# Optimization experiments

Measured on AMD Instinct MI355X. Metric: run time of the kernel, lower is better.

The kernel has to match this reference:

```python
import jax, jax.numpy as jnp
import numpy as np

EMBED_DIM = 2048
NUM_HEADS = 32
NUM_KV_HEADS = 8
HEAD_DIM = EMBED_DIM // NUM_HEADS  # 64
KV_DIM = HEAD_DIM * NUM_KV_HEADS   # 512
Q_PER_KV = NUM_HEADS // NUM_KV_HEADS  # 4


def setup_inputs() -> dict:
    key = jax.random.key(0)
    ks = jax.random.split(key, 9)
    s = 1.0 / np.sqrt(EMBED_DIM)
    x = jax.random.normal(ks[0], (2, 2048, EMBED_DIM), dtype=jnp.float32)
    Wq = jax.random.uniform(ks[1], (EMBED_DIM, EMBED_DIM), jnp.float32, -s, s)
    bq = jax.random.uniform(ks[2], (EMBED_DIM,), jnp.float32, -s, s)
    Wk = jax.random.uniform(ks[3], (KV_DIM, EMBED_DIM), jnp.float32, -s, s)
    bk = jax.random.uniform(ks[4], (KV_DIM,), jnp.float32, -s, s)
    Wv = jax.random.uniform(ks[5], (KV_DIM, EMBED_DIM), jnp.float32, -s, s)
    bv = jax.random.uniform(ks[6], (KV_DIM,), jnp.float32, -s, s)
    Wo = jax.random.uniform(ks[7], (EMBED_DIM, EMBED_DIM), jnp.float32, -s, s)
    bo = jax.random.uniform(ks[8], (EMBED_DIM,), jnp.float32, -s, s)
    return {"x": x, "Wq": Wq, "bq": bq, "Wk": Wk, "bk": bk,
            "Wv": Wv, "bv": bv, "Wo": Wo, "bo": bo}


def reference(x, Wq, bq, Wk, bk, Wv, bv, Wo, bo):
    B, S, E = x.shape
    # projections (torch Linear: x @ W.T + b)
    q = x @ Wq.T + bq                       # [B,S,E]
    k = x @ Wk.T + bk                       # [B,S,KV_DIM]
    v = x @ Wv.T + bv
    # [B, num_kv, q_per_kv, S, D] and [B, num_kv, S, D] -- GQA grouping
    # avoids repeat_interleave duplication while computing identical math
    q = q.reshape(B, S, NUM_KV_HEADS, Q_PER_KV, HEAD_DIM).transpose(0, 2, 3, 1, 4)
    k = k.reshape(B, S, NUM_KV_HEADS, HEAD_DIM).transpose(0, 2, 1, 3)
    v = v.reshape(B, S, NUM_KV_HEADS, HEAD_DIM).transpose(0, 2, 1, 3)
    scale = 1.0 / np.sqrt(HEAD_DIM).astype(np.float32)
    scores = jnp.einsum('bgqsd,bgtd->bgqst', q, k) * scale  # [B,G,Qpk,S,S]
    causal = jnp.triu(jnp.ones((S, S), dtype=bool), k=1)
    scores = jnp.where(causal, jnp.float32(-jnp.inf), scores)
    attn = jax.nn.softmax(scores, axis=-1)
    out = jnp.einsum('bgqst,bgtd->bgqsd', attn, v)          # [B,G,Qpk,S,D]
    # back to [B,S,E]: head order matches repeat_interleave (kv-major)
    out = out.transpose(0, 3, 1, 2, 4).reshape(B, S, E)
    return out @ Wo.T + bo
```

## Files before the change

kernel.cpp:

```cpp
#include <hip/hip_runtime.h>
#include <stdint.h>

#define EMBED  2048
#define SEQ    2048
#define BATCH  2
#define NHEADS 32
#define NKV    8
#define HDIM   64
#define KVD    512
#define MTOT   (BATCH*SEQ)
#define QKVN   (EMBED + 2*KVD)

typedef __bf16 bf16x8 __attribute__((ext_vector_type(8)));
typedef float  f32x4  __attribute__((ext_vector_type(4)));
typedef float  f32x8v __attribute__((ext_vector_type(8)));
typedef float  f32x2v __attribute__((ext_vector_type(2)));
typedef float  f32x16 __attribute__((ext_vector_type(16)));

#define QSCALE 0.18033688f
#define M2     11.541560f

static __device__ __forceinline__ unsigned short f2bf(float f) {
    union { float f; unsigned int u; } v; v.f = f;
    return (unsigned short)((v.u + 0x7fffu + ((v.u >> 16) & 1u)) >> 16);
}

static __device__ __forceinline__ void gload_lds16(const void* g, void* l) {
    __builtin_amdgcn_global_load_lds(
        (const __attribute__((address_space(1))) void*)g,
        (__attribute__((address_space(3))) void*)l, 16, 0, 0);
}

template<int N> static __device__ __forceinline__ void waitvm() {
    if constexpr (N == 2) asm volatile("s_waitcnt vmcnt(2)" ::: "memory");
    else if constexpr (N == 3) asm volatile("s_waitcnt vmcnt(3)" ::: "memory");
    else asm volatile("s_waitcnt vmcnt(4)" ::: "memory");
}

__global__ void cast_f32_bf16(const float* __restrict__ in,
                              unsigned short* __restrict__ out, int n4) {
    int i = blockIdx.x * blockDim.x + threadIdx.x;
    int stride = gridDim.x * blockDim.x;
    for (; i < n4; i += stride) {
        float4 f = reinterpret_cast<const float4*>(in)[i];
        ushort4 o;
        o.x = f2bf(f.x); o.y = f2bf(f.y); o.z = f2bf(f.z); o.w = f2bf(f.w);
        reinterpret_cast<ushort4*>(out)[i] = o;
    }
}

__global__ void pack_bias(const float* __restrict__ bq, const float* __restrict__ bk,
                          const float* __restrict__ bv, float* __restrict__ o) {
    int i = blockIdx.x * blockDim.x + threadIdx.x;
    if (i < EMBED) o[i] = bq[i];
    else if (i < EMBED + KVD) o[i] = bk[i - EMBED];
    else if (i < QKVN) o[i] = bv[i - EMBED - KVD];
}

template<int WM, bool OUT_BF16>
__global__ __launch_bounds__(512, 1)
void gemm8p(const unsigned short* __restrict__ A,
            const unsigned short* __restrict__ B,
            const float* __restrict__ bias,
            void* __restrict__ C, int M, int N, int K)
{
    constexpr int BM    = WM * 32;
    constexpr int ASZ   = BM * 128;
    constexpr int BSZ   = 256 * 128;
    constexpr int AHALF = ASZ / 2;
    constexpr int AL    = AHALF / 8192;
    constexpr int BUFSZ = ASZ + BSZ;

    __shared__ __align__(16) char lds[2 * BUFSZ];

    const int tid = threadIdx.x;
    const int l   = tid & 63;
    const int w   = tid >> 6;
    const int wr  = w >> 2, wc = w & 3;
    const int lr15 = l & 15;
    const int lkb  = (l >> 4) * 16;

    const int nwg = gridDim.x;
    const int cpx = nwg >> 3;
    const int bid = blockIdx.x;
    const int swz = (bid & 7) * cpx + (bid >> 3);
    const int NMB = M / BM;
    const int m0  = (swz % NMB) * BM;
    const int n0  = (swz / NMB) * 256;

    unsigned offA[2][AL], dA[2][AL];
#pragma unroll
    for (int q = 0; q < 2; ++q)
#pragma unroll
        for (int j = 0; j < AL; ++j) {
            int L  = q * AHALF + (tid + j * 512) * 16;
            int R  = L >> 7;
            int cb = (L & 127) ^ ((R & 7) << 4);
            int lrow;
            if constexpr (WM == 8) lrow = ((R >> 6) & 1) * 128 + (R >> 7) * 64 + (R & 63);
            else                   lrow = ((R >> 5) & 1) * 64  + (R >> 6) * 32 + (R & 31);
            offA[q][j] = (unsigned)((m0 + lrow) * K * 2 + cb);
            dA[q][j]   = (unsigned)L;
        }
    unsigned offB[2][2], dB[2][2];
#pragma unroll
    for (int q = 0; q < 2; ++q)
#pragma unroll
        for (int j = 0; j < 2; ++j) {
            int L  = q * 16384 + (tid + j * 512) * 16;
            int R  = L >> 7;
            int cb = (L & 127) ^ ((R & 7) << 4);
            int lrow = ((R >> 5) & 3) * 64 + (R >> 7) * 32 + (R & 31);
            offB[q][j] = (unsigned)((n0 + lrow) * K * 2 + cb);
            dB[q][j]   = (unsigned)(ASZ + L);
        }

#define STAGE_A(q, bw, ku) { _Pragma("unroll") \
    for (int j_ = 0; j_ < AL; ++j_) \
        gload_lds16((const char*)A + offA[q][j_] + (unsigned)(ku) * 128u, (bw) + dA[q][j_]); }
#define STAGE_B(q, bw, ku) { _Pragma("unroll") \
    for (int j_ = 0; j_ < 2; ++j_) \
        gload_lds16((const char*)B + offB[q][j_] + (unsigned)(ku) * 128u, (bw) + dB[q][j_]); }

    auto rdA = [&](const char* br, int mi, int kk) -> bf16x8 {
        int row;
        if constexpr (WM == 8) row = (mi >> 2) * 128 + wr * 64 + (mi & 3) * 16 + lr15;
        else                   row = (mi >> 1) * 64  + wr * 32 + (mi & 1) * 16 + lr15;
        int byte = (row * 128 + kk * 64 + lkb) ^ ((row & 7) << 4);
        return *reinterpret_cast<const bf16x8*>(br + byte);
    };
    auto rdB = [&](const char* br, int ni, int kk) -> bf16x8 {
        int row  = (ni >> 1) * 128 + wc * 32 + (ni & 1) * 16 + lr15;
        int byte = (row * 128 + kk * 64 + lkb) ^ ((row & 7) << 4);
        return *reinterpret_cast<const bf16x8*>(br + ASZ + byte);
    };

    f32x4 acc[WM][4] = {};
    bf16x8 afr[WM / 2][2], bf0[2][2], bf1[2][2];

    STAGE_A(0, lds, 0); STAGE_B(0, lds, 0); STAGE_B(1, lds, 0); STAGE_A(1, lds, 0);
    waitvm<2 + AL>();
    __builtin_amdgcn_s_barrier();

    const int NKT = K >> 6;
    for (int u = 0; u < NKT; ++u) {
        char* br = lds + (u & 1) * BUFSZ;
        char* bw = lds + ((u & 1) ^ 1) * BUFSZ;
        const bool pf = (u + 1 < NKT);
        const int  ku = u + 1;

        if (pf) STAGE_A(0, bw, ku);
#pragma unroll
        for (int mi = 0; mi < WM / 2; ++mi)
#pragma unroll
            for (int kk = 0; kk < 2; ++kk) afr[mi][kk] = rdA(br, mi, kk);
#pragma unroll
        for (int ni = 0; ni < 2; ++ni)
#pragma unroll
            for (int kk = 0; kk < 2; ++kk) bf0[ni][kk] = rdB(br, ni, kk);
        __builtin_amdgcn_s_barrier();
        __builtin_amdgcn_s_setprio(1);
#pragma unroll
        for (int mi = 0; mi < WM / 2; ++mi)
#pragma unroll
            for (int ni = 0; ni < 2; ++ni)
#pragma unroll
                for (int kk = 0; kk < 2; ++kk)
                    acc[mi][ni] = __builtin_amdgcn_mfma_f32_16x16x32_bf16(afr[mi][kk], bf0[ni][kk], acc[mi][ni], 0, 0, 0);
        __builtin_amdgcn_s_setprio(0);
        waitvm<2 * AL>();
        __builtin_amdgcn_s_barrier();

        if (pf) STAGE_B(0, bw, ku);
#pragma unroll
        for (int ni = 0; ni < 2; ++ni)
#pragma unroll
            for (int kk = 0; kk < 2; ++kk) bf1[ni][kk] = rdB(br, 2 + ni, kk);
        __builtin_amdgcn_s_barrier();
        __builtin_amdgcn_s_setprio(1);
#pragma unroll
        for (int mi = 0; mi < WM / 2; ++mi)
#pragma unroll
            for (int ni = 0; ni < 2; ++ni)
#pragma unroll
                for (int kk = 0; kk < 2; ++kk)
                    acc[mi][2 + ni] = __builtin_amdgcn_mfma_f32_16x16x32_bf16(afr[mi][kk], bf1[ni][kk], acc[mi][2 + ni], 0, 0, 0);
        __builtin_amdgcn_s_setprio(0);
        waitvm<AL + 2>();
        __builtin_amdgcn_s_barrier();

        if (pf) STAGE_B(1, bw, ku);
#pragma unroll
        for (int mi = 0; mi < WM / 2; ++mi)
#pragma unroll
            for (int kk = 0; kk < 2; ++kk) afr[mi][kk] = rdA(br, WM / 2 + mi, kk);
        __builtin_amdgcn_s_barrier();
        __builtin_amdgcn_s_setprio(1);
#pragma unroll
        for (int mi = 0; mi < WM / 2; ++mi)
#pragma unroll
            for (int ni = 0; ni < 2; ++ni)
#pragma unroll
                for (int kk = 0; kk < 2; ++kk)
                    acc[WM / 2 + mi][ni] = __builtin_amdgcn_mfma_f32_16x16x32_bf16(afr[mi][kk], bf0[ni][kk], acc[WM / 2 + mi][ni], 0, 0, 0);
        __builtin_amdgcn_s_setprio(0);
        __builtin_amdgcn_s_barrier();

        if (pf) STAGE_A(1, bw, ku);
        __builtin_amdgcn_s_barrier();
        __builtin_amdgcn_s_setprio(1);
#pragma unroll
        for (int mi = 0; mi < WM / 2; ++mi)
#pragma unroll
            for (int ni = 0; ni < 2; ++ni)
#pragma unroll
                for (int kk = 0; kk < 2; ++kk)
                    acc[WM / 2 + mi][2 + ni] = __builtin_amdgcn_mfma_f32_16x16x32_bf16(afr[mi][kk], bf1[ni][kk], acc[WM / 2 + mi][2 + ni], 0, 0, 0);
        __builtin_amdgcn_s_setprio(0);
        waitvm<2 + AL>();
        __builtin_amdgcn_s_barrier();
    }
#undef STAGE_A
#undef STAGE_B

    float bv[4];
#pragma unroll
    for (int ni = 0; ni < 4; ++ni) bv[ni] = bias[n0 + wc * 64 + ni * 16 + lr15];
#pragma unroll
    for (int mi = 0; mi < WM; ++mi)
#pragma unroll
        for (int ni = 0; ni < 4; ++ni)
#pragma unroll
            for (int r = 0; r < 4; ++r) {
                int row = m0 + wr * (WM * 16) + mi * 16 + (l >> 4) * 4 + r;
                int col = n0 + wc * 64 + ni * 16 + lr15;
                float v = acc[mi][ni][r] + bv[ni];
                if constexpr (OUT_BF16)
                    ((unsigned short*)C)[(size_t)row * N + col] = f2bf(v);
                else
                    ((float*)C)[(size_t)row * N + col] = v;
            }
}

static __device__ __forceinline__ bf16x8 pack_frag(float p0, float p1, float p2, float p3,
                                                   float p4, float p5, float p6, float p7) {
    unsigned int w0, w1, w2, w3;
    asm("v_cvt_pk_bf16_f32 %0, %1, %2" : "=v"(w0) : "v"(p0), "v"(p1));
    asm("v_cvt_pk_bf16_f32 %0, %1, %2" : "=v"(w1) : "v"(p2), "v"(p3));
    asm("v_cvt_pk_bf16_f32 %0, %1, %2" : "=v"(w2) : "v"(p4), "v"(p5));
    asm("v_cvt_pk_bf16_f32 %0, %1, %2" : "=v"(w3) : "v"(p6), "v"(p7));
    asm("v_permlane32_swap_b32 %0, %1" : "+v"(w0), "+v"(w2));
    asm("v_permlane32_swap_b32 %0, %1" : "+v"(w1), "+v"(w3));
    union { unsigned int u[4]; bf16x8 v; } uu;
    uu.u[0] = w0; uu.u[1] = w1; uu.u[2] = w2; uu.u[3] = w3;
    return uu.v;
}

static __device__ __forceinline__ float hsum32(f32x16 a, f32x16 b) {
    f32x16 t = a + b;
    f32x8v u = __builtin_shufflevector(t, t, 0,1,2,3,4,5,6,7)
             + __builtin_shufflevector(t, t, 8,9,10,11,12,13,14,15);
    f32x4 v4 = __builtin_shufflevector(u, u, 0,1,2,3)
             + __builtin_shufflevector(u, u, 4,5,6,7);
    f32x2v v2 = __builtin_shufflevector(v4, v4, 0,1)
              + __builtin_shufflevector(v4, v4, 2,3);
    return v2[0] + v2[1];
}

static __device__ __forceinline__ void attn_tile(
    const char* __restrict__ KsBuf, const char* __restrict__ VtBuf,
    const bf16x8* qf, int q, int t0, bool diag,
    f32x16& acc0, f32x16& acc1, float& l_run,
    int lq, int hi)
{
    f32x16 s0 = {}, s1 = {};
    __builtin_amdgcn_s_setprio(1);
#pragma unroll
    for (int ks = 0; ks < 4; ++ks) {
        const int colb = (ks * 16 + hi * 8) * 2;
        int a0 = (lq * 128 + colb) ^ ((lq & 7) << 4);
        bf16x8 kf0 = *reinterpret_cast<const bf16x8*>(KsBuf + a0);
        s0 = __builtin_amdgcn_mfma_f32_32x32x16_bf16(kf0, qf[ks], s0, 0, 0, 0);
        int r1 = 32 + lq;
        int a1 = (r1 * 128 + colb) ^ ((r1 & 7) << 4);
        bf16x8 kf1 = *reinterpret_cast<const bf16x8*>(KsBuf + a1);
        s1 = __builtin_amdgcn_mfma_f32_32x32x16_bf16(kf1, qf[ks], s1, 0, 0, 0);
    }
    __builtin_amdgcn_s_setprio(0);

    if (diag) {
#pragma unroll
        for (int r = 0; r < 16; ++r) {
            int tg = t0 + (r & 3) + 8 * (r >> 2) + 4 * hi;
            if (tg > q) s0[r] = -1e30f;
            if (tg + 32 > q) s1[r] = -1e30f;
        }
    }

    s0 = s0 - M2;
    s1 = s1 - M2;
#pragma unroll
    for (int r = 0; r < 16; ++r) {
        s0[r] = __builtin_amdgcn_exp2f(s0[r]);
        s1[r] = __builtin_amdgcn_exp2f(s1[r]);
    }

    float rs = hsum32(s0, s1);
    l_run += rs + __shfl_xor(rs, 32);

    bf16x8 pa[4];
    pa[0] = pack_frag(s0[0], s0[1], s0[2], s0[3], s0[4], s0[5], s0[6], s0[7]);
    pa[1] = pack_frag(s0[8], s0[9], s0[10], s0[11], s0[12], s0[13], s0[14], s0[15]);
    pa[2] = pack_frag(s1[0], s1[1], s1[2], s1[3], s1[4], s1[5], s1[6], s1[7]);
    pa[3] = pack_frag(s1[8], s1[9], s1[10], s1[11], s1[12], s1[13], s1[14], s1[15]);

    __builtin_amdgcn_s_setprio(1);
#pragma unroll
    for (int ks = 0; ks < 4; ++ks) {
        const int colb = (ks * 16 + hi * 8) * 2;
        int a0 = (lq * 128 + colb) ^ ((lq & 7) << 4);
        bf16x8 vf0 = *reinterpret_cast<const bf16x8*>(VtBuf + a0);
        acc0 = __builtin_amdgcn_mfma_f32_32x32x16_bf16(pa[ks], vf0, acc0, 0, 0, 0);
        int d1 = 32 + lq;
        int a1 = (d1 * 128 + colb) ^ ((d1 & 7) << 4);
        bf16x8 vf1 = *reinterpret_cast<const bf16x8*>(VtBuf + a1);
        acc1 = __builtin_amdgcn_mfma_f32_32x32x16_bf16(pa[ks], vf1, acc1, 0, 0, 0);
    }
    __builtin_amdgcn_s_setprio(0);
}

__global__ __launch_bounds__(512)
void gqa_attn(const unsigned short* __restrict__ qkv,
              unsigned short* __restrict__ ctx)
{
    __shared__ __align__(16) unsigned short Ks[2][64 * 64];
    __shared__ __align__(16) unsigned short Vt[2][64 * 64];

    const int bid = blockIdx.x;
    const int gb  = (bid & 7) * 2 + ((bid >> 3) & 1);
    const int pr  = bid >> 4;
    const int g   = gb & 7;
    const int b   = gb >> 3;
    const int qtA = pr, qtB = 31 - pr;
    const int NT  = qtB + 1;

    const int tid = threadIdx.x;
    const int l   = tid & 63;
    const int w   = tid >> 6;
    const int hi  = l >> 5;
    const int lq  = l & 31;

    const int h   = g * 4 + (w >> 1);
    const int q0A = qtA * 64 + (w & 1) * 32;
    const int q0B = qtB * 64 + (w & 1) * 32;
    const size_t rowb = (size_t)b * SEQ;
    const int kbase = EMBED + g * HDIM;
    const int vbase = EMBED + KVD + g * HDIM;

    bf16x8 qfA[4], qfB[4];
    {
        const char* qa = (const char*)qkv + ((rowb + q0A + lq) * QKVN + (size_t)h * HDIM) * 2;
        const char* qb = (const char*)qkv + ((rowb + q0B + lq) * QKVN + (size_t)h * HDIM) * 2;
#pragma unroll
        for (int ks = 0; ks < 4; ++ks) {
            bf16x8 ta = *reinterpret_cast<const bf16x8*>(qa + (ks * 16 + hi * 8) * 2);
            bf16x8 tb = *reinterpret_cast<const bf16x8*>(qb + (ks * 16 + hi * 8) * 2);
#pragma unroll
            for (int j = 0; j < 8; ++j) {
                ta[j] = (__bf16)((float)ta[j] * QSCALE);
                tb[j] = (__bf16)((float)tb[j] * QSCALE);
            }
            qfA[ks] = ta; qfB[ks] = tb;
        }
    }

    f32x16 accA0 = {}, accA1 = {}, accB0 = {}, accB1 = {};
    float lA = 0.0f, lB = 0.0f;

    const int Lk   = tid << 4;
    const int Tk   = Lk ^ (((Lk >> 7) & 7) << 4);
    const int krow = Tk >> 7, koff = Tk & 127;

    {
        const char* kp = (const char*)qkv + ((rowb + krow) * QKVN + kbase) * 2 + koff;
        gload_lds16(kp, (char*)Ks[0] + Lk);
        const char* vp = (const char*)qkv + ((rowb + l) * QKVN + vbase + w * 8) * 2;
        uint4 vv = *reinterpret_cast<const uint4*>(vp);
        const unsigned short* e = (const unsigned short*)&vv;
#pragma unroll
        for (int j = 0; j < 8; ++j) {
            int d = w * 8 + j;
            int byteoff = (d * 128 + l * 2) ^ ((d & 7) << 4);
            *(unsigned short*)((char*)Vt[0] + byteoff) = e[j];
        }
    }
    __syncthreads();

    for (int kt = 0; kt < NT; ++kt) {
        const int cur = kt & 1;
        const int t0  = kt * 64;
        const bool haveNext = (kt + 1 < NT);
        uint4 vn;
        if (haveNext) {
            const char* kp = (const char*)qkv + ((rowb + t0 + 64 + krow) * QKVN + kbase) * 2 + koff;
            gload_lds16(kp, (char*)Ks[cur ^ 1] + Lk);
            const char* vp = (const char*)qkv + ((rowb + t0 + 64 + l) * QKVN + vbase + w * 8) * 2;
            vn = *reinterpret_cast<const uint4*>(vp);
        }

        attn_tile((const char*)Ks[cur], (const char*)Vt[cur], qfB, q0B + lq, t0,
                  kt == qtB, accB0, accB1, lB, lq, hi);
        if (kt <= qtA)
            attn_tile((const char*)Ks[cur], (const char*)Vt[cur], qfA, q0A + lq, t0,
                      kt == qtA, accA0, accA1, lA, lq, hi);

        if (haveNext) {
            const unsigned short* e = (const unsigned short*)&vn;
#pragma unroll
            for (int j = 0; j < 8; ++j) {
                int d = w * 8 + j;
                int byteoff = (d * 128 + l * 2) ^ ((d & 7) << 4);
                *(unsigned short*)((char*)Vt[cur ^ 1] + byteoff) = e[j];
            }
            __syncthreads();
        }
    }

#pragma unroll
    for (int r = 0; r < 16; ++r) {
        int qr  = (r & 3) + 8 * (r >> 2) + 4 * hi;
        int col = h * HDIM + lq;
        float lrB = __shfl(lB, qr);
        size_t rowB = rowb + q0B + qr;
        ctx[rowB * EMBED + col]      = f2bf(accB0[r] / lrB);
        ctx[rowB * EMBED + col + 32] = f2bf(accB1[r] / lrB);
        float lrA = __shfl(lA, qr);
        size_t rowA = rowb + q0A + qr;
        ctx[rowA * EMBED + col]      = f2bf(accA0[r] / lrA);
        ctx[rowA * EMBED + col + 32] = f2bf(accA1[r] / lrA);
    }
}

extern "C" void kernel_launch(void* const* d_in, const int* in_sizes, int n_in,
                              void* d_out, int out_size, void* d_ws, size_t ws_size,
                              hipStream_t stream) {
    (void)in_sizes; (void)n_in; (void)out_size; (void)ws_size;
    const float* x  = (const float*)d_in[0];
    const float* Wq = (const float*)d_in[1];
    const float* bq = (const float*)d_in[2];
    const float* Wk = (const float*)d_in[3];
    const float* bk = (const float*)d_in[4];
    const float* Wv = (const float*)d_in[5];
    const float* bv = (const float*)d_in[6];
    const float* Wo = (const float*)d_in[7];
    const float* bo = (const float*)d_in[8];
    float* out = (float*)d_out;

    char* ws = (char*)d_ws;
    unsigned short* xb    = (unsigned short*)(ws);
    unsigned short* Wqkvb = (unsigned short*)(ws + 16777216);
    unsigned short* Wob   = (unsigned short*)(ws + 29360128);
    float*          bqkv  = (float*)         (ws + 37748736);
    unsigned short* QKVb  = (unsigned short*)(ws + 37761024);
    unsigned short* ctx   = (unsigned short*)(ws + 62926848);

    cast_f32_bf16<<<2048, 256, 0, stream>>>(x,  xb,                        (MTOT * EMBED) / 4);
    cast_f32_bf16<<<1024, 256, 0, stream>>>(Wq, Wqkvb,                     (EMBED * EMBED) / 4);
    cast_f32_bf16<<<256,  256, 0, stream>>>(Wk, Wqkvb + EMBED * EMBED,     (KVD * EMBED) / 4);
    cast_f32_bf16<<<256,  256, 0, stream>>>(Wv, Wqkvb + (EMBED + KVD) * EMBED, (KVD * EMBED) / 4);
    cast_f32_bf16<<<1024, 256, 0, stream>>>(Wo, Wob,                       (EMBED * EMBED) / 4);
    pack_bias<<<12, 256, 0, stream>>>(bq, bk, bv, bqkv);

    gemm8p<8, true><<<dim3(192), 512, 0, stream>>>(
        xb, Wqkvb, bqkv, QKVb, MTOT, QKVN, EMBED);

    gqa_attn<<<dim3(256), 512, 0, stream>>>(QKVb, ctx);

    gemm8p<4, false><<<dim3(256), 512, 0, stream>>>(
        ctx, Wob, bo, out, MTOT, EMBED, EMBED);
}
```

Measured before the change: 195.9 us.

## Split attention blocks into head pairs with 256 threads and 512 blocks

Each attention block now covers two of the four query heads in a KV group instead of all four. It runs 4 waves instead of 8, and the grid doubles to 512 blocks. Each thread loads twice as much of the K and V tiles, and the launch bounds target 4 blocks per CU. The aim is better CU coverage and occupancy on the large GPU, at the cost of loading each K/V tile twice per group.

```diff
diff --git a/kernel.cpp b/kernel.cpp
--- a/kernel.cpp
+++ b/kernel.cpp
@@ -329,7 +329,7 @@
     __builtin_amdgcn_s_setprio(0);
 }
 
-__global__ __launch_bounds__(512)
+__global__ __launch_bounds__(256, 4)
 void gqa_attn(const unsigned short* __restrict__ qkv,
               unsigned short* __restrict__ ctx)
 {
@@ -337,8 +337,9 @@
     __shared__ __align__(16) unsigned short Vt[2][64 * 64];
 
     const int bid = blockIdx.x;
-    const int gb  = (bid & 7) * 2 + ((bid >> 3) & 1);
-    const int pr  = bid >> 4;
+    const int gb  = bid & 15;
+    const int hp  = (bid >> 4) & 1;
+    const int pr  = bid >> 5;
     const int g   = gb & 7;
     const int b   = gb >> 3;
     const int qtA = pr, qtB = 31 - pr;
@@ -350,7 +351,7 @@
     const int hi  = l >> 5;
     const int lq  = l & 31;
 
-    const int h   = g * 4 + (w >> 1);
+    const int h   = g * 4 + hp * 2 + (w >> 1);
     const int q0A = qtA * 64 + (w & 1) * 32;
     const int q0B = qtB * 64 + (w & 1) * 32;
     const size_t rowb = (size_t)b * SEQ;
@@ -377,21 +378,28 @@
     f32x16 accA0 = {}, accA1 = {}, accB0 = {}, accB1 = {};
     float lA = 0.0f, lB = 0.0f;
 
-    const int Lk   = tid << 4;
-    const int Tk   = Lk ^ (((Lk >> 7) & 7) << 4);
-    const int krow = Tk >> 7, koff = Tk & 127;
+    const int Lk0 = tid << 4;
+    const int Lk1 = (tid + 256) << 4;
+    const int Tk0 = Lk0 ^ (((Lk0 >> 7) & 7) << 4);
+    const int Tk1 = Lk1 ^ (((Lk1 >> 7) & 7) << 4);
+    const int kr0 = Tk0 >> 7, ko0 = Tk0 & 127;
+    const int kr1 = Tk1 >> 7, ko1 = Tk1 & 127;
+
+    const int vd0 = w * 16;
 
     {
-        const char* kp = (const char*)qkv + ((rowb + krow) * QKVN + kbase) * 2 + koff;
-        gload_lds16(kp, (char*)Ks[0] + Lk);
-        const char* vp = (const char*)qkv + ((rowb + l) * QKVN + vbase + w * 8) * 2;
-        uint4 vv = *reinterpret_cast<const uint4*>(vp);
-        const unsigned short* e = (const unsigned short*)&vv;
+        gload_lds16((const char*)qkv + ((rowb + kr0) * QKVN + kbase) * 2 + ko0, (char*)Ks[0] + Lk0);
+        gload_lds16((const char*)qkv + ((rowb + kr1) * QKVN + kbase) * 2 + ko1, (char*)Ks[0] + Lk1);
+        const char* vp = (const char*)qkv + ((rowb + l) * QKVN + vbase + vd0) * 2;
+        uint4 v0 = *reinterpret_cast<const uint4*>(vp);
+        uint4 v1 = *reinterpret_cast<const uint4*>(vp + 16);
+        const unsigned short* e0 = (const unsigned short*)&v0;
+        const unsigned short* e1 = (const unsigned short*)&v1;
 #pragma unroll
         for (int j = 0; j < 8; ++j) {
-            int d = w * 8 + j;
-            int byteoff = (d * 128 + l * 2) ^ ((d & 7) << 4);
-            *(unsigned short*)((char*)Vt[0] + byteoff) = e[j];
+            int d0 = vd0 + j, d1 = vd0 + 8 + j;
+            *(unsigned short*)((char*)Vt[0] + ((d0 * 128 + l * 2) ^ ((d0 & 7) << 4))) = e0[j];
+            *(unsigned short*)((char*)Vt[0] + ((d1 * 128 + l * 2) ^ ((d1 & 7) << 4))) = e1[j];
         }
     }
     __syncthreads();
@@ -400,12 +408,15 @@
         const int cur = kt & 1;
         const int t0  = kt * 64;
         const bool haveNext = (kt + 1 < NT);
-        uint4 vn;
+        uint4 vn0, vn1;
         if (haveNext) {
-            const char* kp = (const char*)qkv + ((rowb + t0 + 64 + krow) * QKVN + kbase) * 2 + koff;
-            gload_lds16(kp, (char*)Ks[cur ^ 1] + Lk);
-            const char* vp = (const char*)qkv + ((rowb + t0 + 64 + l) * QKVN + vbase + w * 8) * 2;
-            vn = *reinterpret_cast<const uint4*>(vp);
+            gload_lds16((const char*)qkv + ((rowb + t0 + 64 + kr0) * QKVN + kbase) * 2 + ko0,
+                        (char*)Ks[cur ^ 1] + Lk0);
+            gload_lds16((const char*)qkv + ((rowb + t0 + 64 + kr1) * QKVN + kbase) * 2 + ko1,
+                        (char*)Ks[cur ^ 1] + Lk1);
+            const char* vp = (const char*)qkv + ((rowb + t0 + 64 + l) * QKVN + vbase + vd0) * 2;
+            vn0 = *reinterpret_cast<const uint4*>(vp);
+            vn1 = *reinterpret_cast<const uint4*>(vp + 16);
         }
 
         attn_tile((const char*)Ks[cur], (const char*)Vt[cur], qfB, q0B + lq, t0,
@@ -415,12 +426,13 @@
                       kt == qtA, accA0, accA1, lA, lq, hi);
 
         if (haveNext) {
-            const unsigned short* e = (const unsigned short*)&vn;
+            const unsigned short* e0 = (const unsigned short*)&vn0;
+            const unsigned short* e1 = (const unsigned short*)&vn1;
 #pragma unroll
             for (int j = 0; j < 8; ++j) {
-                int d = w * 8 + j;
-                int byteoff = (d * 128 + l * 2) ^ ((d & 7) << 4);
-                *(unsigned short*)((char*)Vt[cur ^ 1] + byteoff) = e[j];
+                int d0 = vd0 + j, d1 = vd0 + 8 + j;
+                *(unsigned short*)((char*)Vt[cur ^ 1] + ((d0 * 128 + l * 2) ^ ((d0 & 7) << 4))) = e0[j];
+                *(unsigned short*)((char*)Vt[cur ^ 1] + ((d1 * 128 + l * 2) ^ ((d1 & 7) << 4))) = e1[j];
             }
             __syncthreads();
         }
@@ -474,7 +486,7 @@
     gemm8p<8, true><<<dim3(192), 512, 0, stream>>>(
         xb, Wqkvb, bqkv, QKVb, MTOT, QKVN, EMBED);
 
-    gqa_attn<<<dim3(256), 512, 0, stream>>>(QKVb, ctx);
+    gqa_attn<<<dim3(512), 256, 0, stream>>>(QKVb, ctx);
 
     gemm8p<4, false><<<dim3(256), 512, 0, stream>>>(
         ctx, Wob, bo, out, MTOT, EMBED, EMBED);
```

New measurement: 314.3 us. 1.6x slower.
